# Kernel tuning notes

Measured on AMD Instinct MI355X. Metric: run time of the kernel, lower is better.

The kernel has to match this reference:

```python
import math
import jax, jax.numpy as jnp
import numpy as np

B, T, C = 1, 4096, 2048
H, HKV, D = 16, 4, 128
ROPE_DIM = 128
ROPE_BASE = 500000.0
RMS_EPS = 1e-05
CHUNK = 2048
FFN_H = 8192


def rmsnorm(x, w, eps=RMS_EPS):
    var = jnp.mean(x * x, axis=-1, keepdims=True)
    return x * jax.lax.rsqrt(var + eps) * w


def rope_apply(q, k, rd=ROPE_DIM, base=ROPE_BASE):
    # q, k: [B, H, T, D]; rotate the first rd dims with interleaved pairs.
    b, h, t, d = q.shape
    rd = min(rd, d)
    inv_freq = 1.0 / (base ** (jnp.arange(0, rd, 2, dtype=jnp.float32) / rd))
    pos = jnp.arange(t, dtype=jnp.float32)
    freqs = pos[:, None] * inv_freq[None, :]              # [T, rd//2]
    cos = jnp.cos(freqs)[None, None]                      # [1,1,T,rd//2]
    sin = jnp.sin(freqs)[None, None]

    def _apply(x):
        x1 = x[..., :rd].reshape(b, x.shape[1], t, rd // 2, 2)
        a, bb = x1[..., 0], x1[..., 1]
        a2 = a * cos - bb * sin
        b3 = a * sin + bb * cos
        y1 = jnp.stack([a2, b3], axis=-1).reshape(b, x.shape[1], t, rd)
        return jnp.concatenate([y1, x[..., rd:]], axis=-1)

    return _apply(q), _apply(k)


def chunked_attention(q, k, v, attn_bias, chunk_size=CHUNK):
    # q,k,v: [B,H,T,D]; attn_bias broadcastable to [B,H,T,T].
    b, h, t, d = q.shape
    scale = 1.0 / math.sqrt(d)
    nc = t // chunk_size
    # [nc, B, H, cs, D]
    qc = q.reshape(b, h, nc, chunk_size, d).transpose(2, 0, 1, 3, 4)
    bias = jnp.broadcast_to(attn_bias, attn_bias.shape[:2] + (t, t))
    bc = bias.reshape(bias.shape[0], bias.shape[1], nc, chunk_size, t).transpose(2, 0, 1, 3, 4)

    def one_chunk(args):
        qs, bs = args
        s = jnp.einsum('bhqd,bhkd->bhqk', qs, k) * scale + bs
        p = jax.nn.softmax(s.astype(jnp.float32), axis=-1).astype(q.dtype)
        return jnp.einsum('bhqk,bhkd->bhqd', p, v)

    oc = jax.lax.map(one_chunk, (qc, bc))                 # [nc,B,H,cs,D]
    return oc.transpose(1, 2, 0, 3, 4).reshape(b, h, t, d)


def l4_block(x, attn_bias, attn_norm_w, wq, wk, wv, wo,
             ffn_norm_w, w_gate, w_up, w_down):
    b, t, c = x.shape
    h = rmsnorm(x, attn_norm_w)
    q = (h @ wq.T).reshape(b, t, H, D).transpose(0, 2, 1, 3)    # [B,H,T,D]
    k = (h @ wk.T).reshape(b, t, HKV, D).transpose(0, 2, 1, 3)  # [B,HKV,T,D]
    v = (h @ wv.T).reshape(b, t, HKV, D).transpose(0, 2, 1, 3)
    q, k = rope_apply(q, k)
    rep = H // HKV
    k = jnp.repeat(k, rep, axis=1)                              # GQA expand
    v = jnp.repeat(v, rep, axis=1)
    y = chunked_attention(q, k, v, attn_bias)
    y = y.transpose(0, 2, 1, 3).reshape(b, t, H * D)
    x = x + y @ wo.T
    h2 = rmsnorm(x, ffn_norm_w)
    ffn = (jax.nn.silu(h2 @ w_gate.T) * (h2 @ w_up.T)) @ w_down.T
    return x + ffn


def setup_inputs() -> dict:
    key = jax.random.key(0)
    ks = jax.random.split(key, 9)
    std = 0.02
    x = jax.random.normal(ks[0], (B, T, C), dtype=jnp.float32)
    causal = jnp.triu(jnp.ones((T, T), dtype=bool), k=1)
    attn_bias = jnp.where(causal, jnp.float32(-1e9), jnp.float32(0.0))[None, None]
    return {
        'x': x,
        'attn_bias': attn_bias,
        'attn_norm_w': jnp.ones((C,), jnp.float32),
        'wq': jax.random.normal(ks[1], (H * D, C), jnp.float32) * std,
        'wk': jax.random.normal(ks[2], (HKV * D, C), jnp.float32) * std,
        'wv': jax.random.normal(ks[3], (HKV * D, C), jnp.float32) * std,
        'wo': jax.random.normal(ks[4], (C, H * D), jnp.float32) * std,
        'ffn_norm_w': jnp.ones((C,), jnp.float32),
        'w_gate': jax.random.normal(ks[5], (FFN_H, C), jnp.float32) * std,
        'w_up': jax.random.normal(ks[6], (FFN_H, C), jnp.float32) * std,
        'w_down': jax.random.normal(ks[7], (C, FFN_H), jnp.float32) * std,
    }


def reference(x, attn_bias, attn_norm_w, wq, wk, wv, wo,
              ffn_norm_w, w_gate, w_up, w_down):
    return l4_block(x, attn_bias, attn_norm_w, wq, wk, wv, wo,
                    ffn_norm_w, w_gate, w_up, w_down)
```

## Files before the change

kernel.cpp:

```cpp
#include <hip/hip_runtime.h>
#include <math.h>

#define DEVI static __device__ __forceinline__

typedef __attribute__((ext_vector_type(8))) short bf16x8;
typedef __attribute__((ext_vector_type(4))) short bf16x4;
typedef __attribute__((ext_vector_type(8))) unsigned short ushort8;
typedef __attribute__((ext_vector_type(4))) unsigned short us4;
typedef __attribute__((ext_vector_type(4))) float f32x4;

DEVI unsigned short f32_bf16(float f) {
  unsigned int u = __float_as_uint(f);
  u += 0x7fffu + ((u >> 16) & 1u);
  return (unsigned short)(u >> 16);
}
DEVI float bf16_f32(unsigned short h) {
  return __uint_as_float(((unsigned int)h) << 16);
}

DEVI void async16(void* lds, const void* g) {
  __builtin_amdgcn_global_load_lds(
      (const __attribute__((address_space(1))) void*)g,
      (__attribute__((address_space(3))) void*)lds,
      16, 0, 0);
}

#if __has_builtin(__builtin_amdgcn_mfma_f32_16x16x16bf16_1k)
DEVI f32x4 mfma16(bf16x4 a, bf16x4 b, f32x4 c) {
  return __builtin_amdgcn_mfma_f32_16x16x16bf16_1k(a, b, c, 0, 0, 0);
}
#else
DEVI f32x4 mfma16(bf16x4 a, bf16x4 b, f32x4 c) {
  asm volatile("v_mfma_f32_16x16x16_bf16 %0, %1, %2, %0" : "+v"(c) : "v"(a), "v"(b));
  return c;
}
#endif

__global__ __launch_bounds__(256) void cast_bf16_kernel(
    const float* __restrict__ src, unsigned short* __restrict__ dst, long n8) {
  long i = (long)blockIdx.x * 256 + threadIdx.x;
  if (i >= n8) return;
  const float4 a = *(const float4*)(src + i * 8);
  const float4 b = *(const float4*)(src + i * 8 + 4);
  ushort8 o;
  o[0] = f32_bf16(a.x); o[1] = f32_bf16(a.y); o[2] = f32_bf16(a.z); o[3] = f32_bf16(a.w);
  o[4] = f32_bf16(b.x); o[5] = f32_bf16(b.y); o[6] = f32_bf16(b.z); o[7] = f32_bf16(b.w);
  *(ushort8*)(dst + i * 8) = o;
}

__global__ __launch_bounds__(256) void cast_gu_kernel(
    const float* __restrict__ gate, const float* __restrict__ up,
    unsigned short* __restrict__ dst) {
  long i = (long)blockIdx.x * 256 + threadIdx.x;
  long row = i >> 8;
  long col = (i & 255) * 8;
  const float* src = ((row & 1) ? up : gate) + ((row >> 1) << 11) + col;
  const float4 a = *(const float4*)(src);
  const float4 b = *(const float4*)(src + 4);
  ushort8 o;
  o[0] = f32_bf16(a.x); o[1] = f32_bf16(a.y); o[2] = f32_bf16(a.z); o[3] = f32_bf16(a.w);
  o[4] = f32_bf16(b.x); o[5] = f32_bf16(b.y); o[6] = f32_bf16(b.z); o[7] = f32_bf16(b.w);
  *(ushort8*)(dst + i * 8) = o;
}

__global__ __launch_bounds__(256) void rope_table_kernel(float2* __restrict__ tab) {
  int idx = blockIdx.x * 256 + threadIdx.x;
  int t = idx >> 6, i = idx & 63;
  float inv = __expf(-(float)(2 * i) * (1.0f / 128.0f) * 13.122363377404328f);
  float f = (float)t * inv;
  tab[idx] = make_float2(cosf(f), sinf(f));
}

__global__ __launch_bounds__(256) void rope_apply_kernel(
    unsigned short* __restrict__ qkv, const float2* __restrict__ tab) {
  const int row = blockIdx.x;
  const int tid = threadIdx.x;
#pragma unroll
  for (int it = 0; it < 5; ++it) {
    int p = tid + it * 256;
    int head = p >> 6, i = p & 63;
    int col = (p < 1024) ? (head * 128 + 2 * i) : (2048 + (head - 16) * 128 + 2 * i);
    unsigned short* ptr = qkv + (long)row * 3072 + col;
    float a = bf16_f32(ptr[0]), b = bf16_f32(ptr[1]);
    float2 cs = tab[row * 64 + i];
    float a2 = a * cs.x - b * cs.y;
    float b2 = a * cs.y + b * cs.x;
    ptr[0] = f32_bf16(a2);
    ptr[1] = f32_bf16(b2);
  }
}

__global__ __launch_bounds__(256) void rmsnorm_kernel(
    const float* __restrict__ x, const float* __restrict__ wgt,
    unsigned short* __restrict__ out) {
  __shared__ float red[4];
  const int row = blockIdx.x;
  const int tid = threadIdx.x;
  const float* xr = x + (long)row * 2048 + tid * 8;
  const float4 v0 = *(const float4*)(xr);
  const float4 v1 = *(const float4*)(xr + 4);
  float ss = v0.x * v0.x + v0.y * v0.y + v0.z * v0.z + v0.w * v0.w +
             v1.x * v1.x + v1.y * v1.y + v1.z * v1.z + v1.w * v1.w;
#pragma unroll
  for (int off = 1; off < 64; off <<= 1) ss += __shfl_xor(ss, off);
  if ((tid & 63) == 0) red[tid >> 6] = ss;
  __syncthreads();
  float tot = red[0] + red[1] + red[2] + red[3];
  float sc = rsqrtf(tot * (1.0f / 2048.0f) + 1e-5f);
  const float4 w0 = *(const float4*)(wgt + tid * 8);
  const float4 w1 = *(const float4*)(wgt + tid * 8 + 4);
  ushort8 o;
  o[0] = f32_bf16(v0.x * sc * w0.x); o[1] = f32_bf16(v0.y * sc * w0.y);
  o[2] = f32_bf16(v0.z * sc * w0.z); o[3] = f32_bf16(v0.w * sc * w0.w);
  o[4] = f32_bf16(v1.x * sc * w1.x); o[5] = f32_bf16(v1.y * sc * w1.y);
  o[6] = f32_bf16(v1.z * sc * w1.z); o[7] = f32_bf16(v1.w * sc * w1.w);
  *(ushort8*)(out + (long)row * 2048 + tid * 8) = o;
}

template <int BN, int EPI>
__global__ __launch_bounds__(512, 2) void gemm8p(
    const unsigned short* __restrict__ A, const unsigned short* __restrict__ B,
    void* __restrict__ Cout, const float* __restrict__ res, int M, int N, int K) {
  constexpr int WN = (BN == 256) ? 4 : 2;
  constexpr int WM = 8 / WN;
  constexpr int WTM = 256 / WM;
  constexpr int WTN = BN / WN;
  constexpr int MF = WTM / 16;
  constexpr int NF = WTN / 16;
  constexpr int MFH = MF / 2, NFH = NF / 2;
  constexpr int B_LOADS = (BN * 8) / 512;

  __shared__ __align__(16) unsigned short As[2][256 * 64];
  __shared__ __align__(16) unsigned short Bs[2][BN * 64];

  const int tid = threadIdx.x;
  const int lane = tid & 63;
  const int w = tid >> 6;
  const int c = lane & 15, g = lane >> 4;
  const int c7 = c & 7;
  const int wm = (w / WN) * WTM, wn = (w % WN) * WTN;

  const int id = blockIdx.y * gridDim.x + blockIdx.x;
  const int cpx = (gridDim.x * gridDim.y) >> 3;
  const int sid = (id & 7) * cpx + (id >> 3);
  const int bx = sid % gridDim.x;
  const int by = sid / gridDim.x;
  const long m0 = (long)bx * 256;
  const long n0 = (long)by * BN;

  const f32x4 fzero = {0.f, 0.f, 0.f, 0.f};
  f32x4 acc[MF][NF];
#pragma unroll
  for (int i = 0; i < MF; ++i)
#pragma unroll
    for (int j = 0; j < NF; ++j) acc[i][j] = fzero;

  auto stageA = [&](int buf, int k0) {
#pragma unroll
    for (int q = 0; q < 4; ++q) {
      int G = q * 512 + tid;
      int r = G >> 3;
      int cg = (G & 7) ^ (r & 7);
      async16(&As[buf][(q * 512 + (tid & ~63)) * 8],
              A + (m0 + r) * (long)K + k0 + cg * 8);
    }
  };
  auto stageB = [&](int buf, int k0) {
#pragma unroll
    for (int q = 0; q < B_LOADS; ++q) {
      int G = q * 512 + tid;
      int r = G >> 3;
      int cg = (G & 7) ^ (r & 7);
      async16(&Bs[buf][(q * 512 + (tid & ~63)) * 8],
              B + (n0 + r) * (long)K + k0 + cg * 8);
    }
  };

  stageA(0, 0);
  stageB(0, 0);
  asm volatile("s_waitcnt vmcnt(0)" ::: "memory");
  __builtin_amdgcn_s_barrier();

  const int NT = K >> 6;
  const int swz0 = (g ^ c7) << 3;
  const int swz1 = ((4 + g) ^ c7) << 3;

  for (int t = 0; t < NT; ++t) {
    const int cur = t & 1;
    const unsigned short* Ab = As[cur];
    const unsigned short* Bb = Bs[cur];
#pragma unroll
    for (int ph = 0; ph < 4; ++ph) {
      const int mh = ph >> 1, nh = ph & 1;
      bf16x8 af[MFH][2], bfr[NFH][2];
#pragma unroll
      for (int mf = 0; mf < MFH; ++mf) {
        const int row = wm + (mh * MFH + mf) * 16 + c;
        af[mf][0] = *(const bf16x8*)(Ab + row * 64 + swz0);
        af[mf][1] = *(const bf16x8*)(Ab + row * 64 + swz1);
      }
#pragma unroll
      for (int nf = 0; nf < NFH; ++nf) {
        const int row = wn + (nh * NFH + nf) * 16 + c;
        bfr[nf][0] = *(const bf16x8*)(Bb + row * 64 + swz0);
        bfr[nf][1] = *(const bf16x8*)(Bb + row * 64 + swz1);
      }
      if (t + 1 < NT) {
        if (ph == 0) stageA(cur ^ 1, (t + 1) * 64);
        if (ph == 1) stageB(cur ^ 1, (t + 1) * 64);
      }
      __builtin_amdgcn_s_barrier();
      asm volatile("s_waitcnt lgkmcnt(0)" ::: "memory");
      __builtin_amdgcn_sched_barrier(0);
      __builtin_amdgcn_s_setprio(1);
#pragma unroll
      for (int kk = 0; kk < 2; ++kk)
#pragma unroll
        for (int mf = 0; mf < MFH; ++mf)
#pragma unroll
          for (int nf = 0; nf < NFH; ++nf)
            acc[mh * MFH + mf][nh * NFH + nf] =
                __builtin_amdgcn_mfma_f32_16x16x32_bf16(
                    af[mf][kk], bfr[nf][kk], acc[mh * MFH + mf][nh * NFH + nf],
                    0, 0, 0);
      __builtin_amdgcn_s_setprio(0);
      if (ph == 3) asm volatile("s_waitcnt vmcnt(0)" ::: "memory");
      __builtin_amdgcn_s_barrier();
    }
  }

#pragma unroll
  for (int i = 0; i < MF; ++i) {
#pragma unroll
    for (int j = 0; j < NF; ++j) {
      const long row0 = m0 + wm + i * 16 + g * 4;
      const long col = n0 + wn + j * 16 + c;
#pragma unroll
      for (int r = 0; r < 4; ++r) {
        float v = acc[i][j][r];
        if (EPI == 0) {
          ((unsigned short*)Cout)[(row0 + r) * N + col] = f32_bf16(v);
        } else if (EPI == 1) {
          ((float*)Cout)[(row0 + r) * N + col] = res[(row0 + r) * N + col] + v;
        } else {
          float other = __shfl_xor(v, 1);
          if (!(c & 1)) {
            float sg = v / (1.0f + __expf(-v));
            ((unsigned short*)Cout)[(row0 + r) * (long)(N >> 1) + (col >> 1)] =
                f32_bf16(sg * other);
          }
        }
      }
    }
  }
}

__global__ __launch_bounds__(256) void transpose_v(
    const unsigned short* __restrict__ qkv, unsigned short* __restrict__ vT) {
  __shared__ __align__(16) unsigned short tile[64][72];
  const int tx = blockIdx.x;
  const int dx = blockIdx.y;
  const int tid = threadIdx.x;
  const int r = tid >> 3, cg = tid & 7;
#pragma unroll
  for (int it = 0; it < 2; ++it) {
    const unsigned short* src =
        qkv + (long)(tx * 64 + r + it * 32) * 3072 + 2560 + dx * 64 + cg * 8;
    *(ushort8*)(&tile[r + it * 32][cg * 8]) = *(const ushort8*)src;
  }
  __syncthreads();
#pragma unroll
  for (int it = 0; it < 2; ++it) {
    int d = r + it * 32;
    ushort8 v;
#pragma unroll
    for (int j = 0; j < 8; ++j) v[j] = tile[cg * 8 + j][d];
    *(ushort8*)(vT + (long)(dx * 64 + d) * 4096 + tx * 64 + cg * 8) = v;
  }
}

__global__ __launch_bounds__(512, 2) void attn_kernel(
    const unsigned short* __restrict__ qkv, const unsigned short* __restrict__ vT,
    unsigned short* __restrict__ y) {
  constexpr float SCL = 0.08838834764831845f * 1.4426950408889634f;
  __shared__ __align__(16) unsigned short Kb[2][64 * 128];
  __shared__ __align__(16) unsigned short Vb[2][128 * 64];

  const int tid = threadIdx.x;
  const int lane = tid & 63;
  const int w = tid >> 6;
  const int c = lane & 15, g = lane >> 4;
  const int h = blockIdx.x >> 4;
  const int pid = blockIdx.x & 15;
  const int kvh = h >> 2;
  const int qt = (w < 4) ? pid : (31 - pid);
  const int q0w = qt * 128 + (w & 3) * 32;
  const int nsteps = 2 * (31 - pid) + 2;

  const f32x4 fzero = {0.f, 0.f, 0.f, 0.f};

  bf16x8 qf[2][4];
#pragma unroll
  for (int mt = 0; mt < 2; ++mt)
#pragma unroll
    for (int kk = 0; kk < 4; ++kk)
      qf[mt][kk] = *(const bf16x8*)(qkv + (long)(q0w + mt * 16 + c) * 3072 +
                                    h * 128 + kk * 32 + g * 8);

  f32x4 o[2][8];
#pragma unroll
  for (int mt = 0; mt < 2; ++mt)
#pragma unroll
    for (int dt = 0; dt < 8; ++dt) o[mt][dt] = fzero;
  float m[2] = {-1e30f, -1e30f}, l[2] = {0.f, 0.f};

  auto stage = [&](int buf, int kv0) {
#pragma unroll
    for (int k = 0; k < 2; ++k) {
      int G = k * 512 + tid;
      int row = G >> 4, colg = (G & 15) ^ (row & 7);
      async16(&Kb[buf][(k * 512 + (tid & ~63)) * 8],
              qkv + (long)(kv0 + row) * 3072 + 2048 + kvh * 128 + colg * 8);
    }
#pragma unroll
    for (int k = 0; k < 2; ++k) {
      int G = k * 512 + tid;
      int row = G >> 3, colg = (G & 7) ^ (row & 7);
      async16(&Vb[buf][(k * 512 + (tid & ~63)) * 8],
              vT + (long)(kvh * 128 + row) * 4096 + kv0 + colg * 8);
    }
  };

  stage(0, 0);
  for (int s = 0; s < nsteps; ++s) {
    const int kv0 = s * 64;
    const int bi = s & 1;
    if (s + 1 < nsteps) {
      stage(bi ^ 1, kv0 + 64);
      asm volatile("s_waitcnt vmcnt(4)" ::: "memory");
    } else {
      asm volatile("s_waitcnt vmcnt(0)" ::: "memory");
    }
    __builtin_amdgcn_s_barrier();
    if (kv0 <= q0w + 31) {
      const unsigned short* Ks = Kb[bi];
      const unsigned short* Vs = Vb[bi];
      f32x4 sv[2][4];
#pragma unroll
      for (int mt = 0; mt < 2; ++mt)
#pragma unroll
        for (int nt = 0; nt < 4; ++nt) sv[mt][nt] = fzero;
#pragma unroll
      for (int kk = 0; kk < 4; ++kk) {
        bf16x8 kf[4];
#pragma unroll
        for (int nt = 0; nt < 4; ++nt)
          kf[nt] = *(const bf16x8*)(Ks + (nt * 16 + c) * 128 +
                                    (((kk * 4 + g) ^ (c & 7)) << 3));
#pragma unroll
        for (int mt = 0; mt < 2; ++mt)
#pragma unroll
          for (int nt = 0; nt < 4; ++nt)
            sv[mt][nt] = __builtin_amdgcn_mfma_f32_16x16x32_bf16(
                kf[nt], qf[mt][kk], sv[mt][nt], 0, 0, 0);
      }
      const bool need_mask = (kv0 + 63 > q0w);
      float al[2];
#pragma unroll
      for (int mt = 0; mt < 2; ++mt) {
        const int qrow = q0w + mt * 16 + c;
#pragma unroll
        for (int nt = 0; nt < 4; ++nt)
#pragma unroll
          for (int r = 0; r < 4; ++r) {
            float xx = sv[mt][nt][r] * SCL;
            if (need_mask && (kv0 + nt * 16 + g * 4 + r > qrow)) xx = -3.0e38f;
            sv[mt][nt][r] = xx;
          }
        float mx = -3.0e38f;
#pragma unroll
        for (int nt = 0; nt < 4; ++nt)
#pragma unroll
          for (int r = 0; r < 4; ++r) mx = fmaxf(mx, sv[mt][nt][r]);
        mx = fmaxf(mx, __shfl_xor(mx, 16));
        mx = fmaxf(mx, __shfl_xor(mx, 32));
        const float mn = fmaxf(m[mt], mx);
        const float a = exp2f(m[mt] - mn);
        m[mt] = mn;
        al[mt] = a;
        float rs = 0.f;
#pragma unroll
        for (int nt = 0; nt < 4; ++nt)
#pragma unroll
          for (int r = 0; r < 4; ++r) {
            float p = exp2f(sv[mt][nt][r] - mn);
            sv[mt][nt][r] = p;
            rs += p;
          }
        rs += __shfl_xor(rs, 16);
        rs += __shfl_xor(rs, 32);
        l[mt] = l[mt] * a + rs;
#pragma unroll
        for (int dt = 0; dt < 8; ++dt) o[mt][dt] *= al[mt];
      }
#pragma unroll
      for (int nt = 0; nt < 4; ++nt) {
        bf16x4 pb[2];
#pragma unroll
        for (int mt = 0; mt < 2; ++mt) {
          int lo_, hi_;
          float s0 = sv[mt][nt][0], s1 = sv[mt][nt][1];
          float s2 = sv[mt][nt][2], s3 = sv[mt][nt][3];
          asm("v_cvt_pk_bf16_f32 %0, %1, %2" : "=v"(lo_) : "v"(s0), "v"(s1));
          asm("v_cvt_pk_bf16_f32 %0, %1, %2" : "=v"(hi_) : "v"(s2), "v"(s3));
          int2 pk = make_int2(lo_, hi_);
          pb[mt] = __builtin_bit_cast(bf16x4, pk);
        }
#pragma unroll
        for (int dt = 0; dt < 8; ++dt) {
          bf16x4 vt = *(const bf16x4*)(Vs + (dt * 16 + c) * 64 +
                                       (((nt * 2 + (g >> 1)) ^ (c & 7)) << 3) +
                                       (g & 1) * 4);
          o[0][dt] = mfma16(vt, pb[0], o[0][dt]);
          o[1][dt] = mfma16(vt, pb[1], o[1][dt]);
        }
      }
    }
    __builtin_amdgcn_s_barrier();
  }
#pragma unroll
  for (int mt = 0; mt < 2; ++mt) {
    const float inv = 1.0f / l[mt];
    const long qrow = q0w + mt * 16 + c;
#pragma unroll
    for (int dt = 0; dt < 8; ++dt) {
      us4 st;
      st[0] = f32_bf16(o[mt][dt][0] * inv);
      st[1] = f32_bf16(o[mt][dt][1] * inv);
      st[2] = f32_bf16(o[mt][dt][2] * inv);
      st[3] = f32_bf16(o[mt][dt][3] * inv);
      *(us4*)(y + qrow * 2048 + h * 128 + dt * 16 + g * 4) = st;
    }
  }
}

extern "C" void kernel_launch(void* const* d_in, const int* in_sizes, int n_in,
                              void* d_out, int out_size, void* d_ws, size_t ws_size,
                              hipStream_t stream) {
  (void)in_sizes; (void)n_in; (void)out_size; (void)ws_size;
  const float* x      = (const float*)d_in[0];
  const float* attn_w = (const float*)d_in[2];
  const float* wq     = (const float*)d_in[3];
  const float* wk     = (const float*)d_in[4];
  const float* wv     = (const float*)d_in[5];
  const float* wo     = (const float*)d_in[6];
  const float* ffn_w  = (const float*)d_in[7];
  const float* wg     = (const float*)d_in[8];
  const float* wu     = (const float*)d_in[9];
  const float* wd     = (const float*)d_in[10];
  float* out = (float*)d_out;

  char* ws = (char*)d_ws;
  size_t off = 0;
  auto alloc = [&](size_t bytes) {
    char* p = ws + off;
    off += (bytes + 255) & ~(size_t)255;
    return p;
  };
  float2* rope_tab        = (float2*)alloc(4096UL * 64 * sizeof(float2));
  unsigned short* wqkv_b  = (unsigned short*)alloc(3072UL * 2048 * 2);
  unsigned short* wo_b    = (unsigned short*)alloc(2048UL * 2048 * 2);
  unsigned short* wgu_b   = (unsigned short*)alloc(16384UL * 2048 * 2);
  unsigned short* wd_b    = (unsigned short*)alloc(2048UL * 8192 * 2);
  unsigned short* h_b     = (unsigned short*)alloc(4096UL * 2048 * 2);
  unsigned short* qkv_b   = (unsigned short*)alloc(4096UL * 3072 * 2);
  unsigned short* vT_b    = (unsigned short*)alloc(512UL * 4096 * 2);
  unsigned short* y_b     = (unsigned short*)alloc(4096UL * 2048 * 2);
  float* r1               = (float*)alloc(4096UL * 2048 * 4);
  unsigned short* t_b     = (unsigned short*)alloc(4096UL * 8192 * 2);

  cast_bf16_kernel<<<2048, 256, 0, stream>>>(wq, wqkv_b, 524288);
  cast_bf16_kernel<<<512, 256, 0, stream>>>(wk, wqkv_b + 2048L * 2048, 131072);
  cast_bf16_kernel<<<512, 256, 0, stream>>>(wv, wqkv_b + 2560L * 2048, 131072);
  cast_bf16_kernel<<<2048, 256, 0, stream>>>(wo, wo_b, 524288);
  cast_gu_kernel<<<16384, 256, 0, stream>>>(wg, wu, wgu_b);
  cast_bf16_kernel<<<8192, 256, 0, stream>>>(wd, wd_b, 2097152);
  rope_table_kernel<<<1024, 256, 0, stream>>>(rope_tab);

  rmsnorm_kernel<<<4096, 256, 0, stream>>>(x, attn_w, h_b);
  {
    dim3 grid(16, 12);
    gemm8p<256, 0><<<grid, 512, 0, stream>>>(h_b, wqkv_b, qkv_b, nullptr, 4096, 3072, 2048);
  }
  rope_apply_kernel<<<4096, 256, 0, stream>>>(qkv_b, rope_tab);
  {
    dim3 grid(64, 8);
    transpose_v<<<grid, 256, 0, stream>>>(qkv_b, vT_b);
  }
  attn_kernel<<<256, 512, 0, stream>>>(qkv_b, vT_b, y_b);
  {
    dim3 grid(16, 16);
    gemm8p<128, 1><<<grid, 512, 0, stream>>>(y_b, wo_b, r1, x, 4096, 2048, 2048);
  }

  rmsnorm_kernel<<<4096, 256, 0, stream>>>(r1, ffn_w, h_b);
  {
    dim3 grid(16, 64);
    gemm8p<256, 2><<<grid, 512, 0, stream>>>(h_b, wgu_b, t_b, nullptr, 4096, 16384, 2048);
  }
  {
    dim3 grid(16, 16);
    gemm8p<128, 1><<<grid, 512, 0, stream>>>(t_b, wd_b, out, r1, 4096, 2048, 8192);
  }
}
```

Baseline: 986.5 us.

## Triple-buffer GEMM LDS with two-stage-ahead prefetch and fixed 128-wide N tiles

```diff
diff --git a/kernel.cpp b/kernel.cpp
--- a/kernel.cpp
+++ b/kernel.cpp
@@ -117,28 +117,19 @@
   *(ushort8*)(out + (long)row * 2048 + tid * 8) = o;
 }
 
-template <int BN, int EPI>
+template <int EPI>
 __global__ __launch_bounds__(512, 2) void gemm8p(
     const unsigned short* __restrict__ A, const unsigned short* __restrict__ B,
     void* __restrict__ Cout, const float* __restrict__ res, int M, int N, int K) {
-  constexpr int WN = (BN == 256) ? 4 : 2;
-  constexpr int WM = 8 / WN;
-  constexpr int WTM = 256 / WM;
-  constexpr int WTN = BN / WN;
-  constexpr int MF = WTM / 16;
-  constexpr int NF = WTN / 16;
-  constexpr int MFH = MF / 2, NFH = NF / 2;
-  constexpr int B_LOADS = (BN * 8) / 512;
-
-  __shared__ __align__(16) unsigned short As[2][256 * 64];
-  __shared__ __align__(16) unsigned short Bs[2][BN * 64];
+  __shared__ __align__(16) unsigned short As[3][256 * 64];
+  __shared__ __align__(16) unsigned short Bs[3][128 * 64];
 
   const int tid = threadIdx.x;
   const int lane = tid & 63;
   const int w = tid >> 6;
   const int c = lane & 15, g = lane >> 4;
   const int c7 = c & 7;
-  const int wm = (w / WN) * WTM, wn = (w % WN) * WTN;
+  const int wm = (w >> 2) * 128, wn = (w & 3) * 32;
 
   const int id = blockIdx.y * gridDim.x + blockIdx.x;
   const int cpx = (gridDim.x * gridDim.y) >> 3;
@@ -146,14 +137,14 @@
   const int bx = sid % gridDim.x;
   const int by = sid / gridDim.x;
   const long m0 = (long)bx * 256;
-  const long n0 = (long)by * BN;
+  const long n0 = (long)by * 128;
 
   const f32x4 fzero = {0.f, 0.f, 0.f, 0.f};
-  f32x4 acc[MF][NF];
-#pragma unroll
-  for (int i = 0; i < MF; ++i)
-#pragma unroll
-    for (int j = 0; j < NF; ++j) acc[i][j] = fzero;
+  f32x4 acc[8][2];
+#pragma unroll
+  for (int i = 0; i < 8; ++i)
+#pragma unroll
+    for (int j = 0; j < 2; ++j) acc[i][j] = fzero;
 
   auto stageA = [&](int buf, int k0) {
 #pragma unroll
@@ -167,7 +158,7 @@
   };
   auto stageB = [&](int buf, int k0) {
 #pragma unroll
-    for (int q = 0; q < B_LOADS; ++q) {
+    for (int q = 0; q < 2; ++q) {
       int G = q * 512 + tid;
       int r = G >> 3;
       int cg = (G & 7) ^ (r & 7);
@@ -176,38 +167,41 @@
     }
   };
 
+  const int NT = K >> 6;
   stageA(0, 0);
   stageB(0, 0);
-  asm volatile("s_waitcnt vmcnt(0)" ::: "memory");
+  stageA(1, 64);
+  stageB(1, 64);
+  asm volatile("s_waitcnt vmcnt(6)" ::: "memory");
   __builtin_amdgcn_s_barrier();
 
-  const int NT = K >> 6;
   const int swz0 = (g ^ c7) << 3;
   const int swz1 = ((4 + g) ^ c7) << 3;
 
+  int cur = 0;
   for (int t = 0; t < NT; ++t) {
-    const int cur = t & 1;
     const unsigned short* Ab = As[cur];
     const unsigned short* Bb = Bs[cur];
-#pragma unroll
-    for (int ph = 0; ph < 4; ++ph) {
-      const int mh = ph >> 1, nh = ph & 1;
-      bf16x8 af[MFH][2], bfr[NFH][2];
-#pragma unroll
-      for (int mf = 0; mf < MFH; ++mf) {
-        const int row = wm + (mh * MFH + mf) * 16 + c;
+    const bool pf = (t + 2 < NT);
+    const int nb = (cur >= 1) ? cur - 1 : 2;
+#pragma unroll
+    for (int ph = 0; ph < 2; ++ph) {
+      bf16x8 af[4][2], bfr[2][2];
+#pragma unroll
+      for (int mf = 0; mf < 4; ++mf) {
+        const int row = wm + ph * 64 + mf * 16 + c;
         af[mf][0] = *(const bf16x8*)(Ab + row * 64 + swz0);
         af[mf][1] = *(const bf16x8*)(Ab + row * 64 + swz1);
       }
 #pragma unroll
-      for (int nf = 0; nf < NFH; ++nf) {
-        const int row = wn + (nh * NFH + nf) * 16 + c;
+      for (int nf = 0; nf < 2; ++nf) {
+        const int row = wn + nf * 16 + c;
         bfr[nf][0] = *(const bf16x8*)(Bb + row * 64 + swz0);
         bfr[nf][1] = *(const bf16x8*)(Bb + row * 64 + swz1);
       }
-      if (t + 1 < NT) {
-        if (ph == 0) stageA(cur ^ 1, (t + 1) * 64);
-        if (ph == 1) stageB(cur ^ 1, (t + 1) * 64);
+      if (pf) {
+        if (ph == 0) stageA(nb, (t + 2) << 6);
+        else         stageB(nb, (t + 2) << 6);
       }
       __builtin_amdgcn_s_barrier();
       asm volatile("s_waitcnt lgkmcnt(0)" ::: "memory");
@@ -216,23 +210,25 @@
 #pragma unroll
       for (int kk = 0; kk < 2; ++kk)
 #pragma unroll
-        for (int mf = 0; mf < MFH; ++mf)
-#pragma unroll
-          for (int nf = 0; nf < NFH; ++nf)
-            acc[mh * MFH + mf][nh * NFH + nf] =
-                __builtin_amdgcn_mfma_f32_16x16x32_bf16(
-                    af[mf][kk], bfr[nf][kk], acc[mh * MFH + mf][nh * NFH + nf],
-                    0, 0, 0);
+        for (int mf = 0; mf < 4; ++mf)
+#pragma unroll
+          for (int nf = 0; nf < 2; ++nf)
+            acc[ph * 4 + mf][nf] = __builtin_amdgcn_mfma_f32_16x16x32_bf16(
+                af[mf][kk], bfr[nf][kk], acc[ph * 4 + mf][nf], 0, 0, 0);
       __builtin_amdgcn_s_setprio(0);
-      if (ph == 3) asm volatile("s_waitcnt vmcnt(0)" ::: "memory");
+      if (ph == 1 && t + 1 < NT) {
+        if (pf) asm volatile("s_waitcnt vmcnt(6)" ::: "memory");
+        else    asm volatile("s_waitcnt vmcnt(0)" ::: "memory");
+      }
       __builtin_amdgcn_s_barrier();
     }
-  }
-
-#pragma unroll
-  for (int i = 0; i < MF; ++i) {
-#pragma unroll
-    for (int j = 0; j < NF; ++j) {
+    cur = (cur == 2) ? 0 : cur + 1;
+  }
+
+#pragma unroll
+  for (int i = 0; i < 8; ++i) {
+#pragma unroll
+    for (int j = 0; j < 2; ++j) {
       const long row0 = m0 + wm + i * 16 + g * 4;
       const long col = n0 + wn + j * 16 + c;
 #pragma unroll
@@ -489,8 +485,8 @@
 
   rmsnorm_kernel<<<4096, 256, 0, stream>>>(x, attn_w, h_b);
   {
-    dim3 grid(16, 12);
-    gemm8p<256, 0><<<grid, 512, 0, stream>>>(h_b, wqkv_b, qkv_b, nullptr, 4096, 3072, 2048);
+    dim3 grid(16, 24);
+    gemm8p<0><<<grid, 512, 0, stream>>>(h_b, wqkv_b, qkv_b, nullptr, 4096, 3072, 2048);
   }
   rope_apply_kernel<<<4096, 256, 0, stream>>>(qkv_b, rope_tab);
   {
@@ -500,16 +496,16 @@
   attn_kernel<<<256, 512, 0, stream>>>(qkv_b, vT_b, y_b);
   {
     dim3 grid(16, 16);
-    gemm8p<128, 1><<<grid, 512, 0, stream>>>(y_b, wo_b, r1, x, 4096, 2048, 2048);
+    gemm8p<1><<<grid, 512, 0, stream>>>(y_b, wo_b, r1, x, 4096, 2048, 2048);
   }
 
   rmsnorm_kernel<<<4096, 256, 0, stream>>>(r1, ffn_w, h_b);
   {
-    dim3 grid(16, 64);
-    gemm8p<256, 2><<<grid, 512, 0, stream>>>(h_b, wgu_b, t_b, nullptr, 4096, 16384, 2048);
+    dim3 grid(16, 128);
+    gemm8p<2><<<grid, 512, 0, stream>>>(h_b, wgu_b, t_b, nullptr, 4096, 16384, 2048);
   }
   {
     dim3 grid(16, 16);
-    gemm8p<128, 1><<<grid, 512, 0, stream>>>(t_b, wd_b, out, r1, 4096, 2048, 8192);
-  }
-}
+    gemm8p<1><<<grid, 512, 0, stream>>>(t_b, wd_b, out, r1, 4096, 2048, 8192);
+  }
+}
```

New measurement: 956.6 us. 3.0% less time.

## Restructure GEMM into 4-stage BK=32 pipeline with prefetch distance two

Applied to the files above, without the earlier changes.

```diff
diff --git a/kernel.cpp b/kernel.cpp
--- a/kernel.cpp
+++ b/kernel.cpp
@@ -118,27 +118,21 @@
 }
 
 template <int BN, int EPI>
-__global__ __launch_bounds__(512, 2) void gemm8p(
+__global__ __launch_bounds__(512, 2) void gemm_p(
     const unsigned short* __restrict__ A, const unsigned short* __restrict__ B,
     void* __restrict__ Cout, const float* __restrict__ res, int M, int N, int K) {
-  constexpr int WN = (BN == 256) ? 4 : 2;
-  constexpr int WM = 8 / WN;
-  constexpr int WTM = 256 / WM;
-  constexpr int WTN = BN / WN;
-  constexpr int MF = WTM / 16;
-  constexpr int NF = WTN / 16;
-  constexpr int MFH = MF / 2, NFH = NF / 2;
-  constexpr int B_LOADS = (BN * 8) / 512;
-
-  __shared__ __align__(16) unsigned short As[2][256 * 64];
-  __shared__ __align__(16) unsigned short Bs[2][BN * 64];
+  constexpr int MH = (BN == 256) ? 2 : 1;
+  constexpr int MF = MH * 4;
+  constexpr int BL = (BN == 256) ? 2 : 1;
+  __shared__ __align__(16) unsigned short As[4][256 * 32];
+  __shared__ __align__(16) unsigned short Bs[4][BN * 32];
 
   const int tid = threadIdx.x;
   const int lane = tid & 63;
   const int w = tid >> 6;
   const int c = lane & 15, g = lane >> 4;
-  const int c7 = c & 7;
-  const int wm = (w / WN) * WTM, wn = (w % WN) * WTN;
+  const int wm = (BN == 256) ? (w >> 2) * 128 : (w >> 1) * 64;
+  const int wn = (BN == 256) ? (w & 3) * 64 : (w & 1) * 64;
 
   const int id = blockIdx.y * gridDim.x + blockIdx.x;
   const int cpx = (gridDim.x * gridDim.y) >> 3;
@@ -149,90 +143,88 @@
   const long n0 = (long)by * BN;
 
   const f32x4 fzero = {0.f, 0.f, 0.f, 0.f};
-  f32x4 acc[MF][NF];
+  f32x4 acc[MF][4];
 #pragma unroll
   for (int i = 0; i < MF; ++i)
 #pragma unroll
-    for (int j = 0; j < NF; ++j) acc[i][j] = fzero;
+    for (int j = 0; j < 4; ++j) acc[i][j] = fzero;
 
   auto stageA = [&](int buf, int k0) {
 #pragma unroll
-    for (int q = 0; q < 4; ++q) {
+    for (int q = 0; q < 2; ++q) {
       int G = q * 512 + tid;
-      int r = G >> 3;
-      int cg = (G & 7) ^ (r & 7);
       async16(&As[buf][(q * 512 + (tid & ~63)) * 8],
-              A + (m0 + r) * (long)K + k0 + cg * 8);
+              A + (m0 + (G >> 2)) * (long)K + k0 + (G & 3) * 8);
     }
   };
   auto stageB = [&](int buf, int k0) {
 #pragma unroll
-    for (int q = 0; q < B_LOADS; ++q) {
+    for (int q = 0; q < BL; ++q) {
       int G = q * 512 + tid;
-      int r = G >> 3;
-      int cg = (G & 7) ^ (r & 7);
       async16(&Bs[buf][(q * 512 + (tid & ~63)) * 8],
-              B + (n0 + r) * (long)K + k0 + cg * 8);
+              B + (n0 + (G >> 2)) * (long)K + k0 + (G & 3) * 8);
     }
   };
 
+  const int NT = K >> 5;
   stageA(0, 0);
   stageB(0, 0);
-  asm volatile("s_waitcnt vmcnt(0)" ::: "memory");
+  stageA(1, 32);
+  stageB(1, 32);
+  if constexpr (BN == 256)
+    asm volatile("s_waitcnt vmcnt(4)" ::: "memory");
+  else
+    asm volatile("s_waitcnt vmcnt(3)" ::: "memory");
   __builtin_amdgcn_s_barrier();
 
-  const int NT = K >> 6;
-  const int swz0 = (g ^ c7) << 3;
-  const int swz1 = ((4 + g) ^ c7) << 3;
-
   for (int t = 0; t < NT; ++t) {
-    const int cur = t & 1;
-    const unsigned short* Ab = As[cur];
-    const unsigned short* Bb = Bs[cur];
-#pragma unroll
-    for (int ph = 0; ph < 4; ++ph) {
-      const int mh = ph >> 1, nh = ph & 1;
-      bf16x8 af[MFH][2], bfr[NFH][2];
-#pragma unroll
-      for (int mf = 0; mf < MFH; ++mf) {
-        const int row = wm + (mh * MFH + mf) * 16 + c;
-        af[mf][0] = *(const bf16x8*)(Ab + row * 64 + swz0);
-        af[mf][1] = *(const bf16x8*)(Ab + row * 64 + swz1);
+    const int buf = t & 3;
+    const unsigned short* Ab = As[buf];
+    const unsigned short* Bb = Bs[buf];
+    const bool pf = (t + 2 < NT);
+    const int nb = (t + 2) & 3;
+
+    bf16x8 bfr[4];
+#pragma unroll
+    for (int nf = 0; nf < 4; ++nf)
+      bfr[nf] = *(const bf16x8*)(Bb + (wn + nf * 16 + c) * 32 + g * 8);
+
+#pragma unroll
+    for (int mh = 0; mh < MH; ++mh) {
+      bf16x8 af[4];
+#pragma unroll
+      for (int mf = 0; mf < 4; ++mf)
+        af[mf] = *(const bf16x8*)(Ab + (wm + mh * 64 + mf * 16 + c) * 32 + g * 8);
+      if (pf) {
+        if (mh == 0) stageA(nb, (t + 2) << 5);
+        if (mh == MH - 1) stageB(nb, (t + 2) << 5);
       }
-#pragma unroll
-      for (int nf = 0; nf < NFH; ++nf) {
-        const int row = wn + (nh * NFH + nf) * 16 + c;
-        bfr[nf][0] = *(const bf16x8*)(Bb + row * 64 + swz0);
-        bfr[nf][1] = *(const bf16x8*)(Bb + row * 64 + swz1);
-      }
-      if (t + 1 < NT) {
-        if (ph == 0) stageA(cur ^ 1, (t + 1) * 64);
-        if (ph == 1) stageB(cur ^ 1, (t + 1) * 64);
-      }
-      __builtin_amdgcn_s_barrier();
-      asm volatile("s_waitcnt lgkmcnt(0)" ::: "memory");
       __builtin_amdgcn_sched_barrier(0);
       __builtin_amdgcn_s_setprio(1);
 #pragma unroll
-      for (int kk = 0; kk < 2; ++kk)
-#pragma unroll
-        for (int mf = 0; mf < MFH; ++mf)
-#pragma unroll
-          for (int nf = 0; nf < NFH; ++nf)
-            acc[mh * MFH + mf][nh * NFH + nf] =
-                __builtin_amdgcn_mfma_f32_16x16x32_bf16(
-                    af[mf][kk], bfr[nf][kk], acc[mh * MFH + mf][nh * NFH + nf],
-                    0, 0, 0);
+      for (int mf = 0; mf < 4; ++mf)
+#pragma unroll
+        for (int nf = 0; nf < 4; ++nf)
+          acc[mh * 4 + mf][nf] = __builtin_amdgcn_mfma_f32_16x16x32_bf16(
+              af[mf], bfr[nf], acc[mh * 4 + mf][nf], 0, 0, 0);
       __builtin_amdgcn_s_setprio(0);
-      if (ph == 3) asm volatile("s_waitcnt vmcnt(0)" ::: "memory");
-      __builtin_amdgcn_s_barrier();
-    }
+    }
+
+    if (pf) {
+      if constexpr (BN == 256)
+        asm volatile("s_waitcnt vmcnt(4)" ::: "memory");
+      else
+        asm volatile("s_waitcnt vmcnt(3)" ::: "memory");
+    } else {
+      asm volatile("s_waitcnt vmcnt(0)" ::: "memory");
+    }
+    __builtin_amdgcn_s_barrier();
   }
 
 #pragma unroll
   for (int i = 0; i < MF; ++i) {
 #pragma unroll
-    for (int j = 0; j < NF; ++j) {
+    for (int j = 0; j < 4; ++j) {
       const long row0 = m0 + wm + i * 16 + g * 4;
       const long col = n0 + wn + j * 16 + c;
 #pragma unroll
@@ -490,7 +482,7 @@
   rmsnorm_kernel<<<4096, 256, 0, stream>>>(x, attn_w, h_b);
   {
     dim3 grid(16, 12);
-    gemm8p<256, 0><<<grid, 512, 0, stream>>>(h_b, wqkv_b, qkv_b, nullptr, 4096, 3072, 2048);
+    gemm_p<256, 0><<<grid, 512, 0, stream>>>(h_b, wqkv_b, qkv_b, nullptr, 4096, 3072, 2048);
   }
   rope_apply_kernel<<<4096, 256, 0, stream>>>(qkv_b, rope_tab);
   {
@@ -500,16 +492,16 @@
   attn_kernel<<<256, 512, 0, stream>>>(qkv_b, vT_b, y_b);
   {
     dim3 grid(16, 16);
-    gemm8p<128, 1><<<grid, 512, 0, stream>>>(y_b, wo_b, r1, x, 4096, 2048, 2048);
+    gemm_p<128, 1><<<grid, 512, 0, stream>>>(y_b, wo_b, r1, x, 4096, 2048, 2048);
   }
 
   rmsnorm_kernel<<<4096, 256, 0, stream>>>(r1, ffn_w, h_b);
   {
     dim3 grid(16, 64);
-    gemm8p<256, 2><<<grid, 512, 0, stream>>>(h_b, wgu_b, t_b, nullptr, 4096, 16384, 2048);
+    gemm_p<256, 2><<<grid, 512, 0, stream>>>(h_b, wgu_b, t_b, nullptr, 4096, 16384, 2048);
   }
   {
     dim3 grid(16, 16);
-    gemm8p<128, 1><<<grid, 512, 0, stream>>>(t_b, wd_b, out, r1, 4096, 2048, 8192);
-  }
-}
+    gemm_p<128, 1><<<grid, 512, 0, stream>>>(t_b, wd_b, out, r1, 4096, 2048, 8192);
+  }
+}
```

Result: faster. 899.7 us (-8.8%).
